# Kernel optimization log

Measured on AMD Instinct MI355X. Metric: run time of the kernel, lower is better.

Reference implementation:

```python
import jax, jax.numpy as jnp
import numpy as np

U = 100000   # user_count
I = 50000    # item_count
N = U + I    # total nodes in bipartite graph
D = 64       # embedding dim
L = 3        # num_layers
E = 4800000  # nnz of normalized adjacency
B = 8192     # batch size


def setup_inputs() -> dict:
    key = jax.random.key(0)
    ks = jax.random.split(key, 8)
    edge_src = jax.random.randint(ks[0], (E,), 0, N, dtype=jnp.int32)
    edge_dst = jax.random.randint(ks[1], (E,), 0, N, dtype=jnp.int32)
    # normalized adjacency values ~ 1/sqrt(deg_i*deg_j); small positive numbers
    edge_val = jax.random.uniform(ks[2], (E,), dtype=jnp.float32) * (1.0 / 32.0)
    user_emb_w = jax.random.normal(ks[3], (U, D), dtype=jnp.float32) * 0.01
    item_emb_w = jax.random.normal(ks[4], (I, D), dtype=jnp.float32) * 0.01
    batch_user = jax.random.randint(ks[5], (B,), 0, U, dtype=jnp.int32)
    batch_pos_item = jax.random.randint(ks[6], (B,), 0, I, dtype=jnp.int32)
    batch_neg_item = jax.random.randint(ks[7], (B,), 0, I, dtype=jnp.int32)
    return {
        "edge_src": edge_src,
        "edge_dst": edge_dst,
        "edge_val": edge_val,
        "user_emb_w": user_emb_w,
        "item_emb_w": item_emb_w,
        "batch_user": batch_user,
        "batch_pos_item": batch_pos_item,
        "batch_neg_item": batch_neg_item,
    }


def _spmm(edge_src, edge_dst, edge_val, x):
    # out[i] = sum_{e: dst[e]==i} val[e] * x[src[e]]  (sparse A @ x)
    msgs = edge_val[:, None] * x[edge_src]           # [E, D]
    return jax.ops.segment_sum(msgs, edge_dst, num_segments=N)


def _computer(edge_src, edge_dst, edge_val, user_emb_w, item_emb_w):
    all_emb = jnp.concatenate([user_emb_w, item_emb_w], axis=0)  # [N, D]
    acc = all_emb
    cur = all_emb
    for _ in range(L):
        cur = _spmm(edge_src, edge_dst, edge_val, cur)
        acc = acc + cur
    light_out = acc / jnp.float32(L + 1)  # mean over (L+1) layer embeddings
    return light_out[:U], light_out[U:]


def reference(edge_src, edge_dst, edge_val, user_emb_w, item_emb_w,
              batch_user, batch_pos_item, batch_neg_item):
    all_users, all_items = _computer(edge_src, edge_dst, edge_val,
                                     user_emb_w, item_emb_w)
    user = all_users[batch_user]       # [B, D]
    pos = all_items[batch_pos_item]    # [B, D]
    neg = all_items[batch_neg_item]    # [B, D]
    pos_score = jnp.sum(user * pos, axis=1)
    neg_score = jnp.sum(user * neg, axis=1)
    user0 = user_emb_w[batch_user]
    pos0 = item_emb_w[batch_pos_item]
    neg0 = item_emb_w[batch_neg_item]
    reg_loss = (jnp.sum(user0 * user0) + jnp.sum(pos0 * pos0)
                + jnp.sum(neg0 * neg0))
    return pos_score, neg_score, reg_loss
```

## Files before the change

kernel.cpp:

```cpp
#include <hip/hip_runtime.h>

#define D 64
#define BK 256
#define KMAX 1024
#define PCH 6144
#define PEPT 6
#define SLOT 9216
#define NSL 9

static __device__ __forceinline__ unsigned short f2bf(float f) {
    unsigned int u = __float_as_uint(f);
    unsigned int r = (u + 0x7FFFu + ((u >> 16) & 1u)) >> 16;
    return (unsigned short)r;
}
static __device__ __forceinline__ float bflo(unsigned int u) {
    return __uint_as_float(u << 16);
}
static __device__ __forceinline__ float bfhi(unsigned int u) {
    return __uint_as_float(u & 0xFFFF0000u);
}
static __device__ __forceinline__ int2 ld_i2_glc(const int2* p) {
    long long t = __hip_atomic_load((const long long*)p, __ATOMIC_RELAXED,
                                    __HIP_MEMORY_SCOPE_AGENT);
    int2 r;
    r.x = (int)(unsigned)((unsigned long long)t & 0xFFFFFFFFull);
    r.y = (int)(unsigned)((unsigned long long)t >> 32);
    return r;
}

template <bool GLC>
static __device__ __forceinline__ void row_accum(
        int beg, int end, int lane, int q, int lid,
        const int2* __restrict__ cv_ptr, const uint4* __restrict__ xb,
        float& s0, float& s1, float& s2, float& s3,
        float& s4, float& s5, float& s6, float& s7) {
    for (int base = beg; base < end; base += 64) {
        int e = base + lane;
        int c = 0;
        float v = 0.f;
        if (e < end) {
            int2 cv = GLC ? ld_i2_glc(&cv_ptr[e]) : cv_ptr[e];
            c = cv.x;
            v = bfhi((unsigned)cv.y);
        }
        int nq = (min(64, end - base) + 7) >> 3;
        uint4 t0, t1, t2, t3, t4, t5, t6, t7;
        float w0, w1, w2, w3, w4, w5, w6, w7;
        { int cj = __shfl(c, q, 64);      w0 = __shfl(v, q, 64);      t0 = xb[cj * 8 + lid]; }
        if (nq > 1) { int cj = __shfl(c, 8 + q, 64);  w1 = __shfl(v, 8 + q, 64);  t1 = xb[cj * 8 + lid]; }
        if (nq > 2) { int cj = __shfl(c, 16 + q, 64); w2 = __shfl(v, 16 + q, 64); t2 = xb[cj * 8 + lid]; }
        if (nq > 3) { int cj = __shfl(c, 24 + q, 64); w3 = __shfl(v, 24 + q, 64); t3 = xb[cj * 8 + lid]; }
        if (nq > 4) { int cj = __shfl(c, 32 + q, 64); w4 = __shfl(v, 32 + q, 64); t4 = xb[cj * 8 + lid]; }
        if (nq > 5) { int cj = __shfl(c, 40 + q, 64); w5 = __shfl(v, 40 + q, 64); t5 = xb[cj * 8 + lid]; }
        if (nq > 6) { int cj = __shfl(c, 48 + q, 64); w6 = __shfl(v, 48 + q, 64); t6 = xb[cj * 8 + lid]; }
        if (nq > 7) { int cj = __shfl(c, 56 + q, 64); w7 = __shfl(v, 56 + q, 64); t7 = xb[cj * 8 + lid]; }
#define ACC8(W, T) \
        s0 += (W) * bflo((T).x); s1 += (W) * bfhi((T).x); \
        s2 += (W) * bflo((T).y); s3 += (W) * bfhi((T).y); \
        s4 += (W) * bflo((T).z); s5 += (W) * bfhi((T).z); \
        s6 += (W) * bflo((T).w); s7 += (W) * bfhi((T).w);
        { ACC8(w0, t0) }
        if (nq > 1) { ACC8(w1, t1) }
        if (nq > 2) { ACC8(w2, t2) }
        if (nq > 3) { ACC8(w3, t3) }
        if (nq > 4) { ACC8(w4, t4) }
        if (nq > 5) { ACC8(w5, t5) }
        if (nq > 6) { ACC8(w6, t6) }
        if (nq > 7) { ACC8(w7, t7) }
#undef ACC8
    }
#pragma unroll
    for (int off = 32; off >= 8; off >>= 1) {
        s0 += __shfl_xor(s0, off, 64);
        s1 += __shfl_xor(s1, off, 64);
        s2 += __shfl_xor(s2, off, 64);
        s3 += __shfl_xor(s3, off, 64);
        s4 += __shfl_xor(s4, off, 64);
        s5 += __shfl_xor(s5, off, 64);
        s6 += __shfl_xor(s6, off, 64);
        s7 += __shfl_xor(s7, off, 64);
    }
}

__global__ void __launch_bounds__(1024)
prep_kernel(const int* __restrict__ src,
            const int* __restrict__ dst,
            const float* __restrict__ val,
            int* __restrict__ g_pos,
            int2* __restrict__ st,
            int K_, int E_, int PB, int IB,
            const float4* __restrict__ user_w,
            const float4* __restrict__ item_w,
            ushort4* __restrict__ curb,
            int nu4, int n4,
            const int* __restrict__ bu,
            const int* __restrict__ bp,
            const int* __restrict__ bn,
            int* __restrict__ flags,
            int* __restrict__ list,
            int* __restrict__ n_list,
            int U_, int B_) {
    __shared__ int2 stg[PCH];
    __shared__ int cnt[KMAX];
    __shared__ int sh[KMAX];
    __shared__ int gb[KMAX];
    int bid = blockIdx.x;
    int tid = threadIdx.x;
    if (bid < PB) {
        for (int k = tid; k < K_; k += 1024) cnt[k] = 0;
        __syncthreads();
        int b0 = bid * PCH;
        int nc = min(PCH, E_ - b0);
        int myk[PEPT], myr[PEPT], mysrc[PEPT];
        unsigned mypk[PEPT];
#pragma unroll
        for (int e = 0; e < PEPT; ++e) {
            int i = b0 + e * 1024 + tid;
            if (i < E_) {
                int d = dst[i];
                int k = d >> 8;
                myk[e] = k;
                mysrc[e] = src[i];
                mypk[e] = ((unsigned)f2bf(val[i]) << 16) | (unsigned)(d & (BK - 1));
                myr[e] = atomicAdd(&cnt[k], 1);
            } else {
                myk[e] = -1;
            }
        }
        __syncthreads();
        int v = (tid < K_) ? cnt[tid] : 0;
        sh[tid] = v;
        __syncthreads();
        for (int off = 1; off < KMAX; off <<= 1) {
            int t = (tid >= off) ? sh[tid - off] : 0;
            __syncthreads();
            sh[tid] += t;
            __syncthreads();
        }
        if (tid < K_ && v) {
            int lbase = sh[tid] - v;
            gb[tid] = (tid * SLOT + atomicAdd(&g_pos[tid], v)) - lbase;
        }
        __syncthreads();
#pragma unroll
        for (int e = 0; e < PEPT; ++e) {
            int k = myk[e];
            if (k >= 0) {
                int slot = (sh[k] - cnt[k]) + myr[e];
                stg[slot] = make_int2(mysrc[e] | (k << 20), (int)mypk[e]);
            }
        }
        __syncthreads();
        for (int l = tid; l < nc; l += 1024) {
            int2 ev = stg[l];
            int k = (int)((unsigned)ev.x >> 20);
            st[gb[k] + l] = make_int2(ev.x & 0xFFFFF, ev.y);
        }
    } else if (bid < PB + IB) {
        int i = (bid - PB) * 1024 + tid;
        if (i < n4) {
            float4 v = (i < nu4) ? user_w[i] : item_w[i - nu4];
            ushort4 b;
            b.x = f2bf(v.x); b.y = f2bf(v.y); b.z = f2bf(v.z); b.w = f2bf(v.w);
            curb[i] = b;
        }
    } else {
        int t = (bid - PB - IB) * 1024 + tid;
        int node = -1;
        if (t < 3 * B_) {
            if (t < B_)            node = bu[t];
            else if (t < 2 * B_)   node = U_ + bp[t - B_];
            else                   node = U_ + bn[t - 2 * B_];
        }
        int old = 1;
        if (node >= 0) old = atomicExch(&flags[node], 1);
        unsigned long long m = __ballot(old == 0);
        int lane = tid & 63;
        int myoff = __popcll(m & ((1ull << lane) - 1ull));
        int total = __popcll(m);
        int bse = 0;
        if (lane == 0 && total) bse = atomicAdd(n_list, total);
        bse = __shfl(bse, 0, 64);
        if (old == 0) list[bse + myoff] = node;
    }
}

__global__ void __launch_bounds__(1024)
build_l1_kernel(int2* __restrict__ st,
                const int* __restrict__ g_cnt,
                int2* __restrict__ row_span,
                const uint4* __restrict__ xb,
                uint4* __restrict__ nxtb,
                float4* __restrict__ acc,
                const int* __restrict__ flags,
                int N_) {
    __shared__ int ldeg[BK];
    __shared__ int lsc[BK];
    __shared__ int lcur[BK];
    int b = blockIdx.x;
    int tid = threadIdx.x;
    int sbeg = b * SLOT;
    int rbeg = b << 8;
    int cnt = g_cnt[b];
    if (cnt > SLOT) cnt = SLOT;
    if (tid < BK) ldeg[tid] = 0;
    __syncthreads();
    int2 e0, e1, e2, e3, e4, e5, e6, e7, e8;
#define HL(J, EC) { int i = tid + (J) * 1024; \
        EC = (i < cnt) ? st[sbeg + i] : make_int2(0, 0); \
        if (i < cnt) atomicAdd(&ldeg[(unsigned)EC.y & (BK - 1u)], 1); }
    HL(0, e0) HL(1, e1) HL(2, e2) HL(3, e3) HL(4, e4)
    HL(5, e5) HL(6, e6) HL(7, e7) HL(8, e8)
#undef HL
    __syncthreads();
    int v = 0;
    if (tid < BK) {
        v = ldeg[tid];
        lsc[tid] = v;
    }
    __syncthreads();
    for (int off = 1; off < BK; off <<= 1) {
        int t = (tid < BK && tid >= off) ? lsc[tid - off] : 0;
        __syncthreads();
        if (tid < BK) lsc[tid] += t;
        __syncthreads();
    }
    if (tid < BK) {
        int excl = lsc[tid] - v;
        lcur[tid] = excl;
        lsc[tid] = excl;
        int gi = rbeg + tid;
        if (gi < N_) row_span[gi] = make_int2(sbeg + excl, sbeg + excl + v);
    }
    __syncthreads();
#define SC(J, EC) { int i = tid + (J) * 1024; \
        if (i < cnt) { \
            int p = atomicAdd(&lcur[(unsigned)EC.y & (BK - 1u)], 1); \
            st[sbeg + p] = EC; } }
    SC(0, e0) SC(1, e1) SC(2, e2) SC(3, e3) SC(4, e4)
    SC(5, e5) SC(6, e6) SC(7, e7) SC(8, e8)
#undef SC
    __syncthreads();
    int wid = tid >> 6;
    int lane = tid & 63;
    int q = lane >> 3;
    int lid = lane & 7;
    for (int rr = 0; rr < 16; ++rr) {
        int r = wid * 16 + rr;
        int row = rbeg + r;
        if (row >= N_) break;
        int beg = sbeg + lsc[r];
        int end = beg + ldeg[r];
        float s0 = 0, s1 = 0, s2 = 0, s3 = 0, s4 = 0, s5 = 0, s6 = 0, s7 = 0;
        row_accum<true>(beg, end, lane, q, lid, st, xb,
                        s0, s1, s2, s3, s4, s5, s6, s7);
        if (q == 0) {
            uint4 bb;
            bb.x = (unsigned)f2bf(s0) | ((unsigned)f2bf(s1) << 16);
            bb.y = (unsigned)f2bf(s2) | ((unsigned)f2bf(s3) << 16);
            bb.z = (unsigned)f2bf(s4) | ((unsigned)f2bf(s5) << 16);
            bb.w = (unsigned)f2bf(s6) | ((unsigned)f2bf(s7) << 16);
            nxtb[row * 8 + lid] = bb;
            if (flags[row]) {
                float4* ap = acc + row * 16 + lid * 2;
                ap[0] = make_float4(s0, s1, s2, s3);
                ap[1] = make_float4(s4, s5, s6, s7);
            }
        }
    }
}

__global__ void spmm_csr_kernel(const int2* __restrict__ row_span,
                                const int2* __restrict__ col_val,
                                const uint4* __restrict__ xb,
                                uint4* __restrict__ nxtb,
                                float4* __restrict__ acc,
                                const int* __restrict__ flags,
                                int N_) {
    int row = (int)((blockIdx.x * blockDim.x + threadIdx.x) >> 6);
    int lane = threadIdx.x & 63;
    if (row >= N_) return;
    int q = lane >> 3;
    int lid = lane & 7;
    int2 sp = row_span[row];
    float s0 = 0, s1 = 0, s2 = 0, s3 = 0, s4 = 0, s5 = 0, s6 = 0, s7 = 0;
    row_accum<false>(sp.x, sp.y, lane, q, lid, col_val, xb,
                     s0, s1, s2, s3, s4, s5, s6, s7);
    if (q == 0) {
        uint4 b;
        b.x = (unsigned)f2bf(s0) | ((unsigned)f2bf(s1) << 16);
        b.y = (unsigned)f2bf(s2) | ((unsigned)f2bf(s3) << 16);
        b.z = (unsigned)f2bf(s4) | ((unsigned)f2bf(s5) << 16);
        b.w = (unsigned)f2bf(s6) | ((unsigned)f2bf(s7) << 16);
        nxtb[row * 8 + lid] = b;
        if (flags[row]) {
            float4* ap = acc + row * 16 + lid * 2;
            float4 a0 = ap[0];
            a0.x += s0; a0.y += s1; a0.z += s2; a0.w += s3;
            ap[0] = a0;
            float4 a1 = ap[1];
            a1.x += s4; a1.y += s5; a1.z += s6; a1.w += s7;
            ap[1] = a1;
        }
    }
}

__global__ void spmm_rows_kernel(const int2* __restrict__ row_span,
                                 const int2* __restrict__ col_val,
                                 const uint4* __restrict__ xb,
                                 float4* __restrict__ acc,
                                 const int* __restrict__ list,
                                 const int* __restrict__ n_list) {
    int w = (int)((blockIdx.x * blockDim.x + threadIdx.x) >> 6);
    if (w >= *n_list) return;
    int row = list[w];
    int lane = threadIdx.x & 63;
    int q = lane >> 3;
    int lid = lane & 7;
    int2 sp = row_span[row];
    float s0 = 0, s1 = 0, s2 = 0, s3 = 0, s4 = 0, s5 = 0, s6 = 0, s7 = 0;
    row_accum<false>(sp.x, sp.y, lane, q, lid, col_val, xb,
                     s0, s1, s2, s3, s4, s5, s6, s7);
    if (q == 0) {
        float4* ap = acc + row * 16 + lid * 2;
        float4 a0 = ap[0];
        a0.x += s0; a0.y += s1; a0.z += s2; a0.w += s3;
        ap[0] = a0;
        float4 a1 = ap[1];
        a1.x += s4; a1.y += s5; a1.z += s6; a1.w += s7;
        ap[1] = a1;
    }
}

__global__ void final_kernel(const float* __restrict__ acc,
                             const float* __restrict__ user_w,
                             const float* __restrict__ item_w,
                             const int* __restrict__ bu,
                             const int* __restrict__ bp,
                             const int* __restrict__ bn,
                             float* __restrict__ out,
                             float* __restrict__ red,
                             int U_, int B_) {
    __shared__ float pr[4];
    int w = (int)((blockIdx.x * blockDim.x + threadIdx.x) >> 6);
    int lane = threadIdx.x & 63;
    bool valid = (w < B_);
    float ps = 0.f, ns = 0.f, r = 0.f;
    if (valid) {
        int iu = bu[w], ip = bp[w], in_ = bn[w];
        const float scale = 0.25f;
        float u0 = user_w[(long)iu * D + lane];
        float p0 = item_w[(long)ip * D + lane];
        float n0 = item_w[(long)in_ * D + lane];
        float u = (acc[(long)iu * D + lane] + u0) * scale;
        float p = (acc[(long)(U_ + ip) * D + lane] + p0) * scale;
        float g = (acc[(long)(U_ + in_) * D + lane] + n0) * scale;
        ps = u * p;
        ns = u * g;
        r = u0 * u0 + p0 * p0 + n0 * n0;
    }
#pragma unroll
    for (int off = 32; off; off >>= 1) {
        ps += __shfl_down(ps, off, 64);
        ns += __shfl_down(ns, off, 64);
        r  += __shfl_down(r, off, 64);
    }
    if (lane == 0) pr[threadIdx.x >> 6] = r;
    __syncthreads();
    if (threadIdx.x == 0)
        red[blockIdx.x] = pr[0] + pr[1] + pr[2] + pr[3];
    if (valid && lane == 0) {
        out[w] = ps;
        out[B_ + w] = ns;
    }
}

__global__ void reduce_kernel(const float* __restrict__ red,
                              float* __restrict__ out_scalar, int nblk) {
    __shared__ float sh[256];
    float s = 0.f;
    for (int i = threadIdx.x; i < nblk; i += 256) s += red[i];
    sh[threadIdx.x] = s;
    __syncthreads();
    for (int off = 128; off; off >>= 1) {
        if (threadIdx.x < off) sh[threadIdx.x] += sh[threadIdx.x + off];
        __syncthreads();
    }
    if (threadIdx.x == 0) *out_scalar = sh[0];
}

extern "C" void kernel_launch(void* const* d_in, const int* in_sizes, int n_in,
                              void* d_out, int out_size, void* d_ws, size_t ws_size,
                              hipStream_t stream) {
    const int*   edge_src = (const int*)d_in[0];
    const int*   edge_dst = (const int*)d_in[1];
    const float* edge_val = (const float*)d_in[2];
    const float* user_w   = (const float*)d_in[3];
    const float* item_w   = (const float*)d_in[4];
    const int*   bu       = (const int*)d_in[5];
    const int*   bp       = (const int*)d_in[6];
    const int*   bn       = (const int*)d_in[7];

    int E_ = in_sizes[0];
    int U_ = in_sizes[3] / D;
    int I_ = in_sizes[4] / D;
    int B_ = in_sizes[5];
    int N_ = U_ + I_;
    long ND = (long)N_ * D;
    int K_ = (N_ + BK - 1) >> 8;

    char* p = (char*)d_ws;
    int2* st       = (int2*)p;   p += (size_t)K_ * SLOT * sizeof(int2);
    int2* row_span = (int2*)p;   p += (size_t)N_ * sizeof(int2);
    float* red     = (float*)p;  p += 4096 * sizeof(float);
    char* zb = p;
    int*  g_pos    = (int*)p;    p += KMAX * sizeof(int);
    int*  n_list   = (int*)p;    p += 256;
    int*  flags    = (int*)p;    p += (size_t)N_ * sizeof(int);
    size_t zbytes  = (size_t)(p - zb);
    int*  list     = (int*)p;    p += (size_t)3 * B_ * sizeof(int);
    p = (char*)(((uintptr_t)p + 255) & ~(uintptr_t)255);
    float* acc = (float*)p;                  p += ND * sizeof(float);
    unsigned short* curb = (unsigned short*)p; p += ND * sizeof(unsigned short);
    unsigned short* nxtb = (unsigned short*)p;
    float* out = (float*)d_out;

    int n4 = (int)(ND / 4);
    int nu4 = U_ * D / 4;
    int PB = (E_ + PCH - 1) / PCH;
    int IB = (n4 + 1023) / 1024;
    int FB = (3 * B_ + 1023) / 1024;

    hipMemsetAsync(zb, 0, zbytes, stream);
    prep_kernel<<<PB + IB + FB, 1024, 0, stream>>>(
        edge_src, edge_dst, edge_val, g_pos, st, K_, E_, PB, IB,
        (const float4*)user_w, (const float4*)item_w, (ushort4*)curb,
        nu4, n4, bu, bp, bn, flags, list, n_list, U_, B_);
    build_l1_kernel<<<K_, 1024, 0, stream>>>(
        st, g_pos, row_span, (const uint4*)curb, (uint4*)nxtb, (float4*)acc,
        flags, N_);
    spmm_csr_kernel<<<(N_ + 3) / 4, 256, 0, stream>>>(
        row_span, st, (const uint4*)nxtb, (uint4*)curb, (float4*)acc,
        flags, N_);
    spmm_rows_kernel<<<(3 * B_ + 3) / 4, 256, 0, stream>>>(
        row_span, st, (const uint4*)curb, (float4*)acc, list, n_list);
    int nblk = (B_ * 64 + 255) / 256;
    final_kernel<<<nblk, 256, 0, stream>>>(
        acc, user_w, item_w, bu, bp, bn, out, red, U_, B_);
    reduce_kernel<<<1, 256, 0, stream>>>(red, out + 2 * B_, nblk);
}
```

Before: 400.5 us.

## Split fused sort+layer-1 SpMM into separate kernels; fold final reduction into last block

Removes the first SpMM layer from the bucket-sort kernel, so the sort kernel only builds CSR. Layer 1 now runs as a separate spmm_csr_kernel instance that stores into acc instead of accumulating. Layer 1 gets one wave per row with full occupancy instead of 16 rows serialized per wave behind the sort's barriers, and it no longer needs coherent (GLC) loads of freshly written data. The final reduce kernel is merged into final_kernel with a last-block-done atomic counter, saving one launch. The cost is an extra launch and a re-read of the sorted edges from global memory.

```diff
diff --git a/kernel.cpp b/kernel.cpp
--- a/kernel.cpp
+++ b/kernel.cpp
@@ -6,7 +6,6 @@
 #define PCH 6144
 #define PEPT 6
 #define SLOT 9216
-#define NSL 9
 
 static __device__ __forceinline__ unsigned short f2bf(float f) {
     unsigned int u = __float_as_uint(f);
@@ -19,16 +18,7 @@
 static __device__ __forceinline__ float bfhi(unsigned int u) {
     return __uint_as_float(u & 0xFFFF0000u);
 }
-static __device__ __forceinline__ int2 ld_i2_glc(const int2* p) {
-    long long t = __hip_atomic_load((const long long*)p, __ATOMIC_RELAXED,
-                                    __HIP_MEMORY_SCOPE_AGENT);
-    int2 r;
-    r.x = (int)(unsigned)((unsigned long long)t & 0xFFFFFFFFull);
-    r.y = (int)(unsigned)((unsigned long long)t >> 32);
-    return r;
-}
-
-template <bool GLC>
+
 static __device__ __forceinline__ void row_accum(
         int beg, int end, int lane, int q, int lid,
         const int2* __restrict__ cv_ptr, const uint4* __restrict__ xb,
@@ -39,7 +29,7 @@
         int c = 0;
         float v = 0.f;
         if (e < end) {
-            int2 cv = GLC ? ld_i2_glc(&cv_ptr[e]) : cv_ptr[e];
+            int2 cv = cv_ptr[e];
             c = cv.x;
             v = bfhi((unsigned)cv.y);
         }
@@ -186,14 +176,10 @@
 }
 
 __global__ void __launch_bounds__(1024)
-build_l1_kernel(int2* __restrict__ st,
-                const int* __restrict__ g_cnt,
-                int2* __restrict__ row_span,
-                const uint4* __restrict__ xb,
-                uint4* __restrict__ nxtb,
-                float4* __restrict__ acc,
-                const int* __restrict__ flags,
-                int N_) {
+sort_kernel(int2* __restrict__ st,
+            const int* __restrict__ g_cnt,
+            int2* __restrict__ row_span,
+            int N_) {
     __shared__ int ldeg[BK];
     __shared__ int lsc[BK];
     __shared__ int lcur[BK];
@@ -228,7 +214,6 @@
     if (tid < BK) {
         int excl = lsc[tid] - v;
         lcur[tid] = excl;
-        lsc[tid] = excl;
         int gi = rbeg + tid;
         if (gi < N_) row_span[gi] = make_int2(sbeg + excl, sbeg + excl + v);
     }
@@ -240,36 +225,9 @@
     SC(0, e0) SC(1, e1) SC(2, e2) SC(3, e3) SC(4, e4)
     SC(5, e5) SC(6, e6) SC(7, e7) SC(8, e8)
 #undef SC
-    __syncthreads();
-    int wid = tid >> 6;
-    int lane = tid & 63;
-    int q = lane >> 3;
-    int lid = lane & 7;
-    for (int rr = 0; rr < 16; ++rr) {
-        int r = wid * 16 + rr;
-        int row = rbeg + r;
-        if (row >= N_) break;
-        int beg = sbeg + lsc[r];
-        int end = beg + ldeg[r];
-        float s0 = 0, s1 = 0, s2 = 0, s3 = 0, s4 = 0, s5 = 0, s6 = 0, s7 = 0;
-        row_accum<true>(beg, end, lane, q, lid, st, xb,
-                        s0, s1, s2, s3, s4, s5, s6, s7);
-        if (q == 0) {
-            uint4 bb;
-            bb.x = (unsigned)f2bf(s0) | ((unsigned)f2bf(s1) << 16);
-            bb.y = (unsigned)f2bf(s2) | ((unsigned)f2bf(s3) << 16);
-            bb.z = (unsigned)f2bf(s4) | ((unsigned)f2bf(s5) << 16);
-            bb.w = (unsigned)f2bf(s6) | ((unsigned)f2bf(s7) << 16);
-            nxtb[row * 8 + lid] = bb;
-            if (flags[row]) {
-                float4* ap = acc + row * 16 + lid * 2;
-                ap[0] = make_float4(s0, s1, s2, s3);
-                ap[1] = make_float4(s4, s5, s6, s7);
-            }
-        }
-    }
-}
-
+}
+
+template <bool STORE_ACC>
 __global__ void spmm_csr_kernel(const int2* __restrict__ row_span,
                                 const int2* __restrict__ col_val,
                                 const uint4* __restrict__ xb,
@@ -284,8 +242,8 @@
     int lid = lane & 7;
     int2 sp = row_span[row];
     float s0 = 0, s1 = 0, s2 = 0, s3 = 0, s4 = 0, s5 = 0, s6 = 0, s7 = 0;
-    row_accum<false>(sp.x, sp.y, lane, q, lid, col_val, xb,
-                     s0, s1, s2, s3, s4, s5, s6, s7);
+    row_accum(sp.x, sp.y, lane, q, lid, col_val, xb,
+              s0, s1, s2, s3, s4, s5, s6, s7);
     if (q == 0) {
         uint4 b;
         b.x = (unsigned)f2bf(s0) | ((unsigned)f2bf(s1) << 16);
@@ -295,12 +253,17 @@
         nxtb[row * 8 + lid] = b;
         if (flags[row]) {
             float4* ap = acc + row * 16 + lid * 2;
-            float4 a0 = ap[0];
-            a0.x += s0; a0.y += s1; a0.z += s2; a0.w += s3;
-            ap[0] = a0;
-            float4 a1 = ap[1];
-            a1.x += s4; a1.y += s5; a1.z += s6; a1.w += s7;
-            ap[1] = a1;
+            if (STORE_ACC) {
+                ap[0] = make_float4(s0, s1, s2, s3);
+                ap[1] = make_float4(s4, s5, s6, s7);
+            } else {
+                float4 a0 = ap[0];
+                a0.x += s0; a0.y += s1; a0.z += s2; a0.w += s3;
+                ap[0] = a0;
+                float4 a1 = ap[1];
+                a1.x += s4; a1.y += s5; a1.z += s6; a1.w += s7;
+                ap[1] = a1;
+            }
         }
     }
 }
@@ -319,8 +282,8 @@
     int lid = lane & 7;
     int2 sp = row_span[row];
     float s0 = 0, s1 = 0, s2 = 0, s3 = 0, s4 = 0, s5 = 0, s6 = 0, s7 = 0;
-    row_accum<false>(sp.x, sp.y, lane, q, lid, col_val, xb,
-                     s0, s1, s2, s3, s4, s5, s6, s7);
+    row_accum(sp.x, sp.y, lane, q, lid, col_val, xb,
+              s0, s1, s2, s3, s4, s5, s6, s7);
     if (q == 0) {
         float4* ap = acc + row * 16 + lid * 2;
         float4 a0 = ap[0];
@@ -340,8 +303,10 @@
                              const int* __restrict__ bn,
                              float* __restrict__ out,
                              float* __restrict__ red,
-                             int U_, int B_) {
+                             int* __restrict__ done_cnt,
+                             int U_, int B_, int nblk) {
     __shared__ float pr[4];
+    __shared__ int is_last;
     int w = (int)((blockIdx.x * blockDim.x + threadIdx.x) >> 6);
     int lane = threadIdx.x & 63;
     bool valid = (w < B_);
@@ -366,27 +331,29 @@
         r  += __shfl_down(r, off, 64);
     }
     if (lane == 0) pr[threadIdx.x >> 6] = r;
-    __syncthreads();
-    if (threadIdx.x == 0)
-        red[blockIdx.x] = pr[0] + pr[1] + pr[2] + pr[3];
     if (valid && lane == 0) {
         out[w] = ps;
         out[B_ + w] = ns;
     }
-}
-
-__global__ void reduce_kernel(const float* __restrict__ red,
-                              float* __restrict__ out_scalar, int nblk) {
-    __shared__ float sh[256];
-    float s = 0.f;
-    for (int i = threadIdx.x; i < nblk; i += 256) s += red[i];
-    sh[threadIdx.x] = s;
-    __syncthreads();
-    for (int off = 128; off; off >>= 1) {
-        if (threadIdx.x < off) sh[threadIdx.x] += sh[threadIdx.x + off];
-        __syncthreads();
-    }
-    if (threadIdx.x == 0) *out_scalar = sh[0];
+    __syncthreads();
+    if (threadIdx.x == 0) {
+        red[blockIdx.x] = pr[0] + pr[1] + pr[2] + pr[3];
+        __threadfence();
+        is_last = (atomicAdd(done_cnt, 1) == nblk - 1);
+    }
+    __syncthreads();
+    if (is_last) {
+        float s = 0.f;
+        for (int i = threadIdx.x; i < nblk; i += 256)
+            s += __hip_atomic_load(&red[i], __ATOMIC_RELAXED,
+                                   __HIP_MEMORY_SCOPE_AGENT);
+#pragma unroll
+        for (int off = 32; off; off >>= 1) s += __shfl_down(s, off, 64);
+        if (lane == 0) pr[threadIdx.x >> 6] = s;
+        __syncthreads();
+        if (threadIdx.x == 0)
+            out[2 * B_] = pr[0] + pr[1] + pr[2] + pr[3];
+    }
 }
 
 extern "C" void kernel_launch(void* const* d_in, const int* in_sizes, int n_in,
@@ -415,12 +382,13 @@
     float* red     = (float*)p;  p += 4096 * sizeof(float);
     char* zb = p;
     int*  g_pos    = (int*)p;    p += KMAX * sizeof(int);
-    int*  n_list   = (int*)p;    p += 256;
+    int*  n_list   = (int*)p;
+    int*  done_cnt = n_list + 1; p += 256;
     int*  flags    = (int*)p;    p += (size_t)N_ * sizeof(int);
     size_t zbytes  = (size_t)(p - zb);
     int*  list     = (int*)p;    p += (size_t)3 * B_ * sizeof(int);
     p = (char*)(((uintptr_t)p + 255) & ~(uintptr_t)255);
-    float* acc = (float*)p;                  p += ND * sizeof(float);
+    float* acc = (float*)p;                    p += ND * sizeof(float);
     unsigned short* curb = (unsigned short*)p; p += ND * sizeof(unsigned short);
     unsigned short* nxtb = (unsigned short*)p;
     float* out = (float*)d_out;
@@ -436,16 +404,16 @@
         edge_src, edge_dst, edge_val, g_pos, st, K_, E_, PB, IB,
         (const float4*)user_w, (const float4*)item_w, (ushort4*)curb,
         nu4, n4, bu, bp, bn, flags, list, n_list, U_, B_);
-    build_l1_kernel<<<K_, 1024, 0, stream>>>(
-        st, g_pos, row_span, (const uint4*)curb, (uint4*)nxtb, (float4*)acc,
+    sort_kernel<<<K_, 1024, 0, stream>>>(st, g_pos, row_span, N_);
+    spmm_csr_kernel<true><<<(N_ + 3) / 4, 256, 0, stream>>>(
+        row_span, st, (const uint4*)curb, (uint4*)nxtb, (float4*)acc,
         flags, N_);
-    spmm_csr_kernel<<<(N_ + 3) / 4, 256, 0, stream>>>(
+    spmm_csr_kernel<false><<<(N_ + 3) / 4, 256, 0, stream>>>(
         row_span, st, (const uint4*)nxtb, (uint4*)curb, (float4*)acc,
         flags, N_);
     spmm_rows_kernel<<<(3 * B_ + 3) / 4, 256, 0, stream>>>(
         row_span, st, (const uint4*)curb, (float4*)acc, list, n_list);
     int nblk = (B_ * 64 + 255) / 256;
     final_kernel<<<nblk, 256, 0, stream>>>(
-        acc, user_w, item_w, bu, bp, bn, out, red, U_, B_);
-    reduce_kernel<<<1, 256, 0, stream>>>(red, out + 2 * B_, nblk);
-}
+        acc, user_w, item_w, bu, bp, bn, out, red, done_cnt, U_, B_, nblk);
+}
```

Measured after the change: 422.1 us. 1.05x slower.
